# Kernel optimization log

Hardware: AMD Instinct MI355X
Metric: run time of the kernel (lower is better)

## Reference

```python
import jax, jax.numpy as jnp
import numpy as np

N, E, D, L, G, C = 20000, 320000, 512, 6, 64, 10
EPS = 1e-5


def setup_inputs() -> dict:
    key = jax.random.key(0)
    ks = jax.random.split(key, 8)
    s = 0.05  # small init scale to keep activations sane across 6 layers
    x = jax.random.normal(ks[0], (N, D), jnp.float32)
    edge_index = jax.random.randint(ks[1], (2, E), 0, N, jnp.int32)
    batch = jnp.sort(jax.random.randint(ks[2], (N,), 0, G, jnp.int32))
    W_rel = jax.random.normal(ks[3], (L, D, D), jnp.float32) * s
    b_rel = jnp.zeros((L, D), jnp.float32)
    W_root = jax.random.normal(ks[4], (L, D, D), jnp.float32) * s
    gamma = jnp.ones((L, D), jnp.float32)
    beta = jnp.zeros((L, D), jnp.float32)
    lin_w = jax.random.normal(ks[5], (D, C), jnp.float32) * s
    lin_b = jnp.zeros((C,), jnp.float32)
    return {"x": x, "edge_index": edge_index, "batch": batch,
            "W_rel": W_rel, "b_rel": b_rel, "W_root": W_root,
            "gamma": gamma, "beta": beta, "lin_w": lin_w, "lin_b": lin_b}


def reference(x, edge_index, batch, W_rel, b_rel, W_root, gamma, beta, lin_w, lin_b):
    # PyG GraphConv (aggr='add'): out = segment_sum(x[src] -> dst) @ W_rel + b_rel + x @ W_root
    src, dst = edge_index[0], edge_index[1]
    n = x.shape[0]
    for l in range(W_rel.shape[0]):  # 6 structurally identical layers
        agg = jax.ops.segment_sum(x[src], dst, num_segments=n)  # [N, D]
        h = agg @ W_rel[l] + b_rel[l] + x @ W_root[l]
        # BatchNorm1d in training mode: biased batch statistics over nodes
        mu = jnp.mean(h, axis=0)
        var = jnp.mean(jnp.square(h - mu), axis=0)
        x = jax.nn.relu((h - mu) * jax.lax.rsqrt(var + EPS) * gamma[l] + beta[l])
    # global_mean_pool over per-node graph ids
    sums = jax.ops.segment_sum(x, batch, num_segments=G)              # [G, D]
    counts = jax.ops.segment_sum(jnp.ones((n,), x.dtype), batch, num_segments=G)
    pooled = sums / jnp.maximum(counts, 1.0)[:, None]
    return pooled @ lin_w + lin_b  # [G, C]
```

## Files before the change

kernel.cpp:

```cpp
#include <hip/hip_runtime.h>


typedef unsigned short u16;
typedef unsigned int u32;
typedef __attribute__((ext_vector_type(8))) short bf16x8;
typedef __attribute__((ext_vector_type(16))) float f32x16;
typedef __attribute__((ext_vector_type(2))) float f32x2;

#define DFEAT 512
#define KDIM 1024
#define NLAYER 6
#define NGRAPH 64
#define NCLS 10
#define BN_EPS 1e-5f
#define NBUCKET 1024

__device__ __forceinline__ float bf_lo(u32 u) { union { u32 i; float f; } v; v.i = u << 16; return v.f; }
__device__ __forceinline__ float bf_hi(u32 u) { union { u32 i; float f; } v; v.i = u & 0xFFFF0000u; return v.f; }
__device__ __forceinline__ u16 f2bf(float f) {
  union { float f; u32 i; } v; v.f = f;
  u32 r = v.i + 0x7FFFu + ((v.i >> 16) & 1u);
  return (u16)(r >> 16);
}
__device__ __forceinline__ u32 pack2(float lo, float hi) {
  return (u32)f2bf(lo) | ((u32)f2bf(hi) << 16);
}

__device__ __forceinline__ void gload_lds16(const u16* g, u16* lds_base) {
  __builtin_amdgcn_global_load_lds(
      (const __attribute__((address_space(1))) u32*)g,
      (__attribute__((address_space(3))) u32*)lds_base, 16, 0, 0);
}

__global__ void prep_kernel(const int* __restrict__ ei, int* __restrict__ counts, int E,
                            const float* __restrict__ Wrel, const float* __restrict__ Wroot,
                            u16* __restrict__ Wt,
                            const float* __restrict__ x, u16* __restrict__ A, int M,
                            int histB, int wB) {
  __shared__ float tile[64][65];
  int b = blockIdx.x;
  int tid = threadIdx.x;
  if (b < histB) {
    int e = b * 256 + tid;
    if (e < E) atomicAdd(&counts[ei[E + e]], 1);
  } else if (b < histB + wB) {
    int t = b - histB;
    int l = t >> 7;
    int tt = t & 127;
    int k0 = (tt >> 3) << 6;
    int n0 = (tt & 7) << 6;
    int rr = tid >> 4;
    int c4 = (tid & 15) << 2;
#pragma unroll
    for (int i = 0; i < 4; i++) {
      int k = k0 + i * 16 + rr;
      const float* src = (k < DFEAT)
          ? &Wrel[((size_t)l * DFEAT + k) * DFEAT + n0 + c4]
          : &Wroot[((size_t)l * DFEAT + (k - DFEAT)) * DFEAT + n0 + c4];
      float4 v = *(const float4*)src;
      float* d = &tile[i * 16 + rr][c4];
      d[0] = v.x; d[1] = v.y; d[2] = v.z; d[3] = v.w;
    }
    __syncthreads();
    int nr = tid >> 3;
    int kc = (tid & 7) << 3;
#pragma unroll
    for (int i = 0; i < 2; i++) {
      int nl = i * 32 + nr;
      uint4 o;
      o.x = pack2(tile[kc + 0][nl], tile[kc + 1][nl]);
      o.y = pack2(tile[kc + 2][nl], tile[kc + 3][nl]);
      o.z = pack2(tile[kc + 4][nl], tile[kc + 5][nl]);
      o.w = pack2(tile[kc + 6][nl], tile[kc + 7][nl]);
      *(uint4*)&Wt[(size_t)(l * DFEAT + n0 + nl) * KDIM + k0 + kc] = o;
    }
  } else {
    int idx = (b - histB - wB) * 256 + tid;
    int row = idx >> 7;
    int c4 = (idx & 127) * 4;
    if (row < M) {
      float4 v = *(const float4*)&x[(size_t)row * DFEAT + c4];
      uint2 o; o.x = pack2(v.x, v.y); o.y = pack2(v.z, v.w);
      *(uint2*)&A[(size_t)row * KDIM + DFEAT + c4] = o;
    }
  }
}

__global__ __launch_bounds__(1024) void dscan_kernel(const int* __restrict__ counts,
                                                     int* __restrict__ base0,
                                                     int* __restrict__ bcur,
                                                     int* __restrict__ edgebase,
                                                     int* __restrict__ row_ptr2, int n) {
  __shared__ int hist[NBUCKET];
  __shared__ int part[NBUCKET];
  int tid = threadIdx.x;
  hist[tid] = 0;
  __syncthreads();
  for (int i = tid; i < n; i += 1024) {
    int d = counts[i]; if (d > NBUCKET - 1) d = NBUCKET - 1;
    atomicAdd(&hist[d], 1);
  }
  __syncthreads();
  int c = hist[tid];
  part[tid] = c; __syncthreads();
  int x = c;
  for (int off = 1; off < NBUCKET; off <<= 1) {
    int t = (tid >= off) ? part[tid - off] : 0;
    __syncthreads();
    x += t; part[tid] = x;
    __syncthreads();
  }
  base0[tid] = x - c;
  bcur[tid] = x - c;
  int w = c * tid;
  part[tid] = w; __syncthreads();
  int y = w;
  for (int off = 1; off < NBUCKET; off <<= 1) {
    int t = (tid >= off) ? part[tid - off] : 0;
    __syncthreads();
    y += t; part[tid] = y;
    __syncthreads();
  }
  edgebase[tid] = y - w;
  if (tid == NBUCKET - 1) row_ptr2[n] = y;
}

__global__ __launch_bounds__(256) void rank_kernel(const int* __restrict__ counts,
                                                   const int* __restrict__ base0,
                                                   int* __restrict__ bcur,
                                                   const int* __restrict__ edgebase,
                                                   int* __restrict__ perm,
                                                   int* __restrict__ row_ptr2,
                                                   int* __restrict__ cursor2, int n) {
  __shared__ int hb[NBUCKET];
  __shared__ int hstart[NBUCKET];
  int tid = threadIdx.x;
  for (int d = tid; d < NBUCKET; d += 256) hb[d] = 0;
  __syncthreads();
  int row = blockIdx.x * 256 + tid;
  bool valid = (row < n);
  int deg = 0, j = 0;
  if (valid) {
    deg = counts[row]; if (deg > NBUCKET - 1) deg = NBUCKET - 1;
    j = atomicAdd(&hb[deg], 1);
  }
  __syncthreads();
  for (int d = tid; d < NBUCKET; d += 256) {
    int c = hb[d];
    hstart[d] = c ? atomicAdd(&bcur[d], c) : 0;
  }
  __syncthreads();
  if (valid) {
    int rnk = hstart[deg] + j;
    int jj = rnk - base0[deg];
    int v = edgebase[deg] + jj * deg;
    perm[rnk] = row;
    row_ptr2[rnk] = v;
    cursor2[row] = v;
  }
}

__global__ void scatter_kernel(const int* __restrict__ ei, int* __restrict__ cursor2,
                               int* __restrict__ csr2, int E) {
  int e = blockIdx.x * 256 + threadIdx.x;
  if (e < E) {
    int d = ei[E + e];
    int pos = atomicAdd(&cursor2[d], 1);
    csr2[pos] = ei[e];
  }
}

template <bool FUSED>
__device__ __forceinline__ void acc8(uint4 v, const f32x2* sc, const f32x2* sh, f32x2* a) {
  f32x2 t0 = {bf_lo(v.x), bf_hi(v.x)};
  f32x2 t1 = {bf_lo(v.y), bf_hi(v.y)};
  f32x2 t2 = {bf_lo(v.z), bf_hi(v.z)};
  f32x2 t3 = {bf_lo(v.w), bf_hi(v.w)};
  if constexpr (FUSED) {
    f32x2 z = {0.f, 0.f};
    a[0] += __builtin_elementwise_max(t0 * sc[0] + sh[0], z);
    a[1] += __builtin_elementwise_max(t1 * sc[1] + sh[1], z);
    a[2] += __builtin_elementwise_max(t2 * sc[2] + sh[2], z);
    a[3] += __builtin_elementwise_max(t3 * sc[3] + sh[3], z);
  } else {
    a[0] += t0; a[1] += t1; a[2] += t2; a[3] += t3;
  }
}

#define GCAP 1536
template <bool FUSED>
__global__ __launch_bounds__(256) void gather_kernel(u16* __restrict__ A,
                                                     const u16* __restrict__ Hb,
                                                     const float* __restrict__ sums,
                                                     const float* __restrict__ gamma,
                                                     const float* __restrict__ beta,
                                                     const int* __restrict__ row_ptr2,
                                                     const int* __restrict__ csr2,
                                                     const int* __restrict__ perm,
                                                     int n, float invN) {
  __shared__ int sidx[GCAP];
  int b = blockIdx.x;
  int slice = b & 7;
  int nGrp = (n + 31) >> 5;
  int grp = nGrp - 1 - (b >> 3);
  int tid = threadIdx.x;
  int r0 = grp * 32;
  int rend = (r0 + 32 < n) ? (r0 + 32) : n;
  int wbeg = row_ptr2[r0], wend = row_ptr2[rend];
  int cnt = wend - wbeg;
  bool lds_ok = (cnt <= GCAP);
  if (lds_ok)
    for (int t = tid; t < cnt; t += 256) sidx[t] = csr2[wbeg + t];
  __syncthreads();

  int wid = tid >> 6, lane = tid & 63;
  int dsub = lane >> 3, fl = lane & 7;
  int rnk = r0 + wid * 8 + dsub;
  if (rnk >= n) return;
  int dst = perm[rnk];
  int cc = slice * 64 + fl * 8;
  f32x2 sc2[4], sh2[4];
  if constexpr (FUSED) {
#pragma unroll
    for (int j = 0; j < 8; j++) {
      int c = cc + j;
      float mu = sums[c] * invN;
      float var = sums[DFEAT + c] * invN - mu * mu;
      float s = gamma[c] * rsqrtf(var + BN_EPS);
      sc2[j >> 1][j & 1] = s;
      sh2[j >> 1][j & 1] = beta[c] - mu * s;
    }
    uint4 h = *(const uint4*)&Hb[(size_t)dst * DFEAT + cc];
    f32x2 z = {0.f, 0.f};
    f32x2 e0 = __builtin_elementwise_max((f32x2){bf_lo(h.x), bf_hi(h.x)} * sc2[0] + sh2[0], z);
    f32x2 e1 = __builtin_elementwise_max((f32x2){bf_lo(h.y), bf_hi(h.y)} * sc2[1] + sh2[1], z);
    f32x2 e2 = __builtin_elementwise_max((f32x2){bf_lo(h.z), bf_hi(h.z)} * sc2[2] + sh2[2], z);
    f32x2 e3 = __builtin_elementwise_max((f32x2){bf_lo(h.w), bf_hi(h.w)} * sc2[3] + sh2[3], z);
    uint4 o;
    o.x = pack2(e0[0], e0[1]); o.y = pack2(e1[0], e1[1]);
    o.z = pack2(e2[0], e2[1]); o.w = pack2(e3[0], e3[1]);
    *(uint4*)&A[(size_t)dst * KDIM + DFEAT + cc] = o;
  }
  const u16* Sx = FUSED ? (Hb + cc) : (A + DFEAT + cc);
  const size_t RS = FUSED ? DFEAT : KDIM;
  int db = row_ptr2[rnk], de = row_ptr2[rnk + 1];
  f32x2 a[4] = {};
  if (lds_ok) {
    int e = db - wbeg, ee = de - wbeg;
    for (; e + 7 < ee; e += 8) {
      int s0 = sidx[e + 0], s1 = sidx[e + 1], s2 = sidx[e + 2], s3 = sidx[e + 3];
      int s4 = sidx[e + 4], s5 = sidx[e + 5], s6 = sidx[e + 6], s7 = sidx[e + 7];
      uint4 v0 = *(const uint4*)&Sx[(size_t)s0 * RS];
      uint4 v1 = *(const uint4*)&Sx[(size_t)s1 * RS];
      uint4 v2 = *(const uint4*)&Sx[(size_t)s2 * RS];
      uint4 v3 = *(const uint4*)&Sx[(size_t)s3 * RS];
      uint4 v4 = *(const uint4*)&Sx[(size_t)s4 * RS];
      uint4 v5 = *(const uint4*)&Sx[(size_t)s5 * RS];
      uint4 v6 = *(const uint4*)&Sx[(size_t)s6 * RS];
      uint4 v7 = *(const uint4*)&Sx[(size_t)s7 * RS];
      acc8<FUSED>(v0, sc2, sh2, a); acc8<FUSED>(v1, sc2, sh2, a);
      acc8<FUSED>(v2, sc2, sh2, a); acc8<FUSED>(v3, sc2, sh2, a);
      acc8<FUSED>(v4, sc2, sh2, a); acc8<FUSED>(v5, sc2, sh2, a);
      acc8<FUSED>(v6, sc2, sh2, a); acc8<FUSED>(v7, sc2, sh2, a);
    }
    for (; e < ee; ++e) {
      uint4 v = *(const uint4*)&Sx[(size_t)sidx[e] * RS];
      acc8<FUSED>(v, sc2, sh2, a);
    }
  } else {
    for (int e = db; e < de; ++e) {
      uint4 v = *(const uint4*)&Sx[(size_t)csr2[e] * RS];
      acc8<FUSED>(v, sc2, sh2, a);
    }
  }
  uint4 o;
  o.x = pack2(a[0][0], a[0][1]); o.y = pack2(a[1][0], a[1][1]);
  o.z = pack2(a[2][0], a[2][1]); o.w = pack2(a[3][0], a[3][1]);
  *(uint4*)&A[(size_t)dst * KDIM + cc] = o;
}

#define BM 128
#define BN 128
#define BK 64
#define CSTR 132
#define BUFSZ (BM * BK + BN * BK)
__global__ __launch_bounds__(256, 2) void gemm_kernel(const u16* __restrict__ A,
                                                      const u16* __restrict__ Bt,
                                                      const float* __restrict__ bias,
                                                      u16* __restrict__ Hb,
                                                      float* __restrict__ sums, int M) {
  const int lin = blockIdx.x;
  const int bx = ((lin >> 5) << 3) + (lin & 7);
  const int by = (lin >> 3) & 3;
  const int m0 = bx * BM;
  if (m0 >= M) return;
  const int n0 = by * BN;

  __shared__ u16 smem[2 * BUFSZ];
  __shared__ float sred[2 * BN];
  const int tid = threadIdx.x;
  const int wid = tid >> 6, lane = tid & 63;
  const int wm = wid >> 1, wn = wid & 1;
  const int l31 = lane & 31, half = lane >> 5;

  if (tid < 2 * BN) sred[tid] = 0.f;

  const int dr = lane >> 3;
  const int gcol = ((lane & 7) ^ dr) * 8;
  int arow[4], brow[4];
#pragma unroll
  for (int t = 0; t < 4; t++) {
    int r = wid * 32 + t * 8 + dr;
    int ar = m0 + r; if (ar >= M) ar = M - 1;
    arow[t] = ar;
    brow[t] = n0 + r;
  }

  f32x16 acc[2][2] = {};

#pragma unroll
  for (int t = 0; t < 4; t++) {
    gload_lds16(&A[(size_t)arow[t] * KDIM + gcol], &smem[(wid * 32 + t * 8) * BK]);
    gload_lds16(&Bt[(size_t)brow[t] * KDIM + gcol], &smem[BM * BK + (wid * 32 + t * 8) * BK]);
  }
  __syncthreads();

  const int NIT = KDIM / BK;
  for (int it = 0; it < NIT; ++it) {
    const int cur = it & 1;
    if (it + 1 < NIT) {
      const int k1 = (it + 1) * BK;
      u16* Asn = &smem[(cur ^ 1) * BUFSZ];
      u16* Bsn = Asn + BM * BK;
#pragma unroll
      for (int t = 0; t < 4; t++) {
        gload_lds16(&A[(size_t)arow[t] * KDIM + k1 + gcol], &Asn[(wid * 32 + t * 8) * BK]);
        gload_lds16(&Bt[(size_t)brow[t] * KDIM + k1 + gcol], &Bsn[(wid * 32 + t * 8) * BK]);
      }
    }
    const u16* Asc = &smem[cur * BUFSZ];
    const u16* Bsc = Asc + BM * BK;
#pragma unroll
    for (int ks = 0; ks < 4; ks++) {
      int slot = ((ks * 2 + half) ^ (l31 & 7)) * 8;
      bf16x8 a0 = *(const bf16x8*)&Asc[(wm * 64 + l31) * BK + slot];
      bf16x8 a1 = *(const bf16x8*)&Asc[(wm * 64 + 32 + l31) * BK + slot];
      bf16x8 b0 = *(const bf16x8*)&Bsc[(wn * 64 + l31) * BK + slot];
      bf16x8 b1 = *(const bf16x8*)&Bsc[(wn * 64 + 32 + l31) * BK + slot];
      acc[0][0] = __builtin_amdgcn_mfma_f32_32x32x16_bf16(a0, b0, acc[0][0], 0, 0, 0);
      acc[0][1] = __builtin_amdgcn_mfma_f32_32x32x16_bf16(a0, b1, acc[0][1], 0, 0, 0);
      acc[1][0] = __builtin_amdgcn_mfma_f32_32x32x16_bf16(a1, b0, acc[1][0], 0, 0, 0);
      acc[1][1] = __builtin_amdgcn_mfma_f32_32x32x16_bf16(a1, b1, acc[1][1], 0, 0, 0);
    }
    __syncthreads();
  }

#pragma unroll
  for (int nt = 0; nt < 2; nt++) {
    int colt = wn * 64 + nt * 32 + l31;
    float bv = bias[n0 + colt];
    float s = 0.f, s2 = 0.f;
#pragma unroll
    for (int mt = 0; mt < 2; mt++) {
      int rbase = wm * 64 + mt * 32 + half * 4;
#pragma unroll
      for (int reg = 0; reg < 16; reg++) {
        int rowt = rbase + (reg & 3) + 8 * (reg >> 2);
        float v = acc[mt][nt][reg] + bv;
        smem[rowt * CSTR + colt] = f2bf(v);
        if (m0 + rowt < M) { s += v; s2 += v * v; }
      }
    }
    s  += __shfl_xor(s, 32);
    s2 += __shfl_xor(s2, 32);
    if (half == 0) {
      atomicAdd(&sred[colt], s);
      atomicAdd(&sred[BN + colt], s2);
    }
  }
  __syncthreads();

  const int rsub = tid >> 4;
  const int c8 = (tid & 15) * 8;
#pragma unroll
  for (int it = 0; it < 8; it++) {
    int rowt = it * 16 + rsub;
    int grow = m0 + rowt;
    if (grow < M) {
      uint4 v = *(const uint4*)&smem[rowt * CSTR + c8];
      *(uint4*)&Hb[(size_t)grow * DFEAT + n0 + c8] = v;
    }
  }
  if (tid < BN) {
    atomicAdd(&sums[n0 + tid], sred[tid]);
    atomicAdd(&sums[DFEAT + n0 + tid], sred[BN + tid]);
  }
}

__device__ __forceinline__ int lower_bound_dev(const int* a, int n, int v) {
  int lo = 0, hi = n;
  while (lo < hi) { int mid = (lo + hi) >> 1; if (a[mid] < v) lo = mid + 1; else hi = mid; }
  return lo;
}

__global__ __launch_bounds__(1024) void pool_kernel(const u16* __restrict__ Hb,
                                                    const float* __restrict__ sums,
                                                    const float* __restrict__ gamma,
                                                    const float* __restrict__ beta,
                                                    const int* __restrict__ batch,
                                                    float* __restrict__ pooled, int n, float invN) {
  __shared__ float red[DFEAT];
  int g = blockIdx.x;
  int tid = threadIdx.x;
  if (tid < DFEAT) red[tid] = 0.f;
  int lo = lower_bound_dev(batch, n, g);
  int hi = lower_bound_dev(batch, n, g + 1);
  int rowOff = tid >> 6, lane = tid & 63;
  int c0 = lane * 8;
  float sc[8], sh[8];
#pragma unroll
  for (int j = 0; j < 8; j++) {
    int c = c0 + j;
    float mu = sums[c] * invN;
    float var = sums[DFEAT + c] * invN - mu * mu;
    float s = gamma[c] * rsqrtf(var + BN_EPS);
    sc[j] = s;
    sh[j] = beta[c] - mu * s;
  }
  float a[8] = {};
  for (int r = lo + rowOff; r < hi; r += 16) {
    uint4 v = *(const uint4*)&Hb[(size_t)r * DFEAT + c0];
    float e0 = bf_lo(v.x), e1 = bf_hi(v.x), e2 = bf_lo(v.y), e3 = bf_hi(v.y);
    float e4 = bf_lo(v.z), e5 = bf_hi(v.z), e6 = bf_lo(v.w), e7 = bf_hi(v.w);
    a[0] += fmaxf(e0 * sc[0] + sh[0], 0.f); a[1] += fmaxf(e1 * sc[1] + sh[1], 0.f);
    a[2] += fmaxf(e2 * sc[2] + sh[2], 0.f); a[3] += fmaxf(e3 * sc[3] + sh[3], 0.f);
    a[4] += fmaxf(e4 * sc[4] + sh[4], 0.f); a[5] += fmaxf(e5 * sc[5] + sh[5], 0.f);
    a[6] += fmaxf(e6 * sc[6] + sh[6], 0.f); a[7] += fmaxf(e7 * sc[7] + sh[7], 0.f);
  }
  __syncthreads();
#pragma unroll
  for (int j = 0; j < 8; j++) atomicAdd(&red[c0 + j], a[j]);
  __syncthreads();
  if (tid < DFEAT) pooled[g * DFEAT + tid] = red[tid] / fmaxf((float)(hi - lo), 1.0f);
}

__global__ __launch_bounds__(64) void final_kernel(const float* __restrict__ pooled,
                                                   const float* __restrict__ lin_w,
                                                   const float* __restrict__ lin_b,
                                                   float* __restrict__ out) {
  int g = blockIdx.x;
  int lane = threadIdx.x;
  float acc[NCLS] = {};
  float4 p0 = *(const float4*)&pooled[g * DFEAT + lane * 8];
  float4 p1 = *(const float4*)&pooled[g * DFEAT + lane * 8 + 4];
  float pv[8] = {p0.x, p0.y, p0.z, p0.w, p1.x, p1.y, p1.z, p1.w};
#pragma unroll
  for (int j = 0; j < 8; j++) {
    int k = lane * 8 + j;
#pragma unroll
    for (int c = 0; c < NCLS; c++) acc[c] += pv[j] * lin_w[k * NCLS + c];
  }
#pragma unroll
  for (int off = 32; off > 0; off >>= 1)
#pragma unroll
    for (int c = 0; c < NCLS; c++) acc[c] += __shfl_down(acc[c], off);
  if (lane == 0)
#pragma unroll
    for (int c = 0; c < NCLS; c++) out[g * NCLS + c] = acc[c] + lin_b[c];
}

extern "C" void kernel_launch(void* const* d_in, const int* in_sizes, int n_in,
                              void* d_out, int out_size, void* d_ws, size_t ws_size,
                              hipStream_t stream) {
  const float* x      = (const float*)d_in[0];
  const int*   ei     = (const int*)d_in[1];
  const int*   batch  = (const int*)d_in[2];
  const float* W_rel  = (const float*)d_in[3];
  const float* b_rel  = (const float*)d_in[4];
  const float* W_root = (const float*)d_in[5];
  const float* gamma  = (const float*)d_in[6];
  const float* beta   = (const float*)d_in[7];
  const float* lin_w  = (const float*)d_in[8];
  const float* lin_b  = (const float*)d_in[9];
  float* out = (float*)d_out;

  const int N = in_sizes[0] / DFEAT;
  const int E = in_sizes[1] / 2;

  char* p = (char*)d_ws;
  u16*   A        = (u16*)p;    p += (size_t)N * KDIM * 2;
  u16*   Hb       = (u16*)p;    p += (size_t)N * DFEAT * 2;
  u16*   Wt       = (u16*)p;    p += (size_t)NLAYER * DFEAT * KDIM * 2;
  int*   row_ptr2 = (int*)p;    p += ((size_t)(N + 1) * 4 + 15) / 16 * 16;
  int*   counts   = (int*)p;    p += (size_t)N * 4;
  int*   cursor2  = (int*)p;    p += (size_t)N * 4;
  int*   perm     = (int*)p;    p += (size_t)N * 4;
  int*   csr2     = (int*)p;    p += (size_t)E * 4;
  int*   base0    = (int*)p;    p += (size_t)NBUCKET * 4;
  int*   bcur     = (int*)p;    p += (size_t)NBUCKET * 4;
  int*   edgebase = (int*)p;    p += (size_t)NBUCKET * 4;
  float* sums     = (float*)p;  p += (size_t)NLAYER * 2 * DFEAT * 4;
  float* pooled   = (float*)p;  p += (size_t)NGRAPH * DFEAT * 4;

  const float invN = 1.0f / (float)N;

  hipMemsetAsync(counts, 0, (size_t)N * 4, stream);
  hipMemsetAsync(sums, 0, (size_t)NLAYER * 2 * DFEAT * 4, stream);

  const int histB = (E + 255) / 256;
  const int wB = NLAYER * 128;
  const int xB = (N * 128 + 255) / 256;
  prep_kernel<<<histB + wB + xB, 256, 0, stream>>>(ei, counts, E, W_rel, W_root, Wt,
                                                   x, A, N, histB, wB);
  dscan_kernel<<<1, 1024, 0, stream>>>(counts, base0, bcur, edgebase, row_ptr2, N);
  rank_kernel<<<(N + 255) / 256, 256, 0, stream>>>(counts, base0, bcur, edgebase,
                                                   perm, row_ptr2, cursor2, N);
  scatter_kernel<<<(E + 255) / 256, 256, 0, stream>>>(ei, cursor2, csr2, E);

  const int ngrp8 = ((N + 31) / 32) * 8;
  const int gtiles = (((N + BM - 1) / BM + 7) / 8) * 8 * 4;

  for (int l = 0; l < NLAYER; ++l) {
    float* sums_l = sums + (size_t)l * 2 * DFEAT;
    if (l == 0)
      gather_kernel<false><<<ngrp8, 256, 0, stream>>>(A, Hb, nullptr, nullptr, nullptr,
                                                      row_ptr2, csr2, perm, N, invN);
    else
      gather_kernel<true><<<ngrp8, 256, 0, stream>>>(A, Hb,
          sums + (size_t)(l - 1) * 2 * DFEAT,
          gamma + (size_t)(l - 1) * DFEAT, beta + (size_t)(l - 1) * DFEAT,
          row_ptr2, csr2, perm, N, invN);
    gemm_kernel<<<gtiles, 256, 0, stream>>>(A, Wt + (size_t)l * DFEAT * KDIM,
                                            b_rel + (size_t)l * DFEAT, Hb, sums_l, N);
  }

  pool_kernel<<<NGRAPH, 1024, 0, stream>>>(Hb, sums + (size_t)(NLAYER - 1) * 2 * DFEAT,
                                           gamma + (size_t)(NLAYER - 1) * DFEAT,
                                           beta + (size_t)(NLAYER - 1) * DFEAT,
                                           batch, pooled, N, invN);
  final_kernel<<<NGRAPH, 64, 0, stream>>>(pooled, lin_w, lin_b, out);
}
```

Before: 621.7 us.

## Deepen GEMM prefetch to two stages and fuse final linear into pool kernel

```diff
diff --git a/kernel.cpp b/kernel.cpp
--- a/kernel.cpp
+++ b/kernel.cpp
@@ -316,28 +316,30 @@
     brow[t] = n0 + r;
   }
 
+  auto STAGE = [&](int pb, int kt) {
+    const int k0 = kt * BK;
+    u16* As = &smem[pb * BUFSZ];
+    u16* Bs = As + BM * BK;
+#pragma unroll
+    for (int t = 0; t < 4; t++)
+      gload_lds16(&A[(size_t)arow[t] * KDIM + k0 + gcol], &As[(wid * 32 + t * 8) * BK]);
+#pragma unroll
+    for (int t = 0; t < 4; t++)
+      gload_lds16(&Bt[(size_t)brow[t] * KDIM + k0 + gcol], &Bs[(wid * 32 + t * 8) * BK]);
+  };
+
   f32x16 acc[2][2] = {};
 
-#pragma unroll
-  for (int t = 0; t < 4; t++) {
-    gload_lds16(&A[(size_t)arow[t] * KDIM + gcol], &smem[(wid * 32 + t * 8) * BK]);
-    gload_lds16(&Bt[(size_t)brow[t] * KDIM + gcol], &smem[BM * BK + (wid * 32 + t * 8) * BK]);
-  }
-  __syncthreads();
+  STAGE(0, 0);
+  STAGE(1, 1);
+  asm volatile("s_waitcnt vmcnt(8)" ::: "memory");
+  __builtin_amdgcn_sched_barrier(0);
+  __builtin_amdgcn_s_barrier();
+  __builtin_amdgcn_sched_barrier(0);
 
   const int NIT = KDIM / BK;
   for (int it = 0; it < NIT; ++it) {
     const int cur = it & 1;
-    if (it + 1 < NIT) {
-      const int k1 = (it + 1) * BK;
-      u16* Asn = &smem[(cur ^ 1) * BUFSZ];
-      u16* Bsn = Asn + BM * BK;
-#pragma unroll
-      for (int t = 0; t < 4; t++) {
-        gload_lds16(&A[(size_t)arow[t] * KDIM + k1 + gcol], &Asn[(wid * 32 + t * 8) * BK]);
-        gload_lds16(&Bt[(size_t)brow[t] * KDIM + k1 + gcol], &Bsn[(wid * 32 + t * 8) * BK]);
-      }
-    }
     const u16* Asc = &smem[cur * BUFSZ];
     const u16* Bsc = Asc + BM * BK;
 #pragma unroll
@@ -352,7 +354,20 @@
       acc[1][0] = __builtin_amdgcn_mfma_f32_32x32x16_bf16(a1, b0, acc[1][0], 0, 0, 0);
       acc[1][1] = __builtin_amdgcn_mfma_f32_32x32x16_bf16(a1, b1, acc[1][1], 0, 0, 0);
     }
-    __syncthreads();
+    __builtin_amdgcn_sched_barrier(0);
+    __builtin_amdgcn_s_barrier();
+    __builtin_amdgcn_sched_barrier(0);
+    if (it + 2 < NIT) {
+      STAGE(cur, it + 2);
+      asm volatile("s_waitcnt vmcnt(8)" ::: "memory");
+    } else if (it + 2 == NIT) {
+      asm volatile("s_waitcnt vmcnt(0)" ::: "memory");
+    }
+    __builtin_amdgcn_sched_barrier(0);
+    if (it + 1 < NIT) {
+      __builtin_amdgcn_s_barrier();
+      __builtin_amdgcn_sched_barrier(0);
+    }
   }
 
 #pragma unroll
@@ -408,11 +423,15 @@
                                                     const float* __restrict__ gamma,
                                                     const float* __restrict__ beta,
                                                     const int* __restrict__ batch,
-                                                    float* __restrict__ pooled, int n, float invN) {
+                                                    const float* __restrict__ lin_w,
+                                                    const float* __restrict__ lin_b,
+                                                    float* __restrict__ out, int n, float invN) {
   __shared__ float red[DFEAT];
+  __shared__ float outc[NCLS];
   int g = blockIdx.x;
   int tid = threadIdx.x;
   if (tid < DFEAT) red[tid] = 0.f;
+  if (tid >= DFEAT && tid < DFEAT + NCLS) outc[tid - DFEAT] = 0.f;
   int lo = lower_bound_dev(batch, n, g);
   int hi = lower_bound_dev(batch, n, g + 1);
   int rowOff = tid >> 6, lane = tid & 63;
@@ -441,32 +460,22 @@
 #pragma unroll
   for (int j = 0; j < 8; j++) atomicAdd(&red[c0 + j], a[j]);
   __syncthreads();
-  if (tid < DFEAT) pooled[g * DFEAT + tid] = red[tid] / fmaxf((float)(hi - lo), 1.0f);
-}
-
-__global__ __launch_bounds__(64) void final_kernel(const float* __restrict__ pooled,
-                                                   const float* __restrict__ lin_w,
-                                                   const float* __restrict__ lin_b,
-                                                   float* __restrict__ out) {
-  int g = blockIdx.x;
-  int lane = threadIdx.x;
-  float acc[NCLS] = {};
-  float4 p0 = *(const float4*)&pooled[g * DFEAT + lane * 8];
-  float4 p1 = *(const float4*)&pooled[g * DFEAT + lane * 8 + 4];
-  float pv[8] = {p0.x, p0.y, p0.z, p0.w, p1.x, p1.y, p1.z, p1.w};
-#pragma unroll
-  for (int j = 0; j < 8; j++) {
-    int k = lane * 8 + j;
-#pragma unroll
-    for (int c = 0; c < NCLS; c++) acc[c] += pv[j] * lin_w[k * NCLS + c];
-  }
-#pragma unroll
-  for (int off = 32; off > 0; off >>= 1)
-#pragma unroll
-    for (int c = 0; c < NCLS; c++) acc[c] += __shfl_down(acc[c], off);
-  if (lane == 0)
-#pragma unroll
-    for (int c = 0; c < NCLS; c++) out[g * NCLS + c] = acc[c] + lin_b[c];
+  float invCnt = 1.0f / fmaxf((float)(hi - lo), 1.0f);
+  if (tid < DFEAT) {
+    float pv = red[tid] * invCnt;
+    float pc[NCLS];
+#pragma unroll
+    for (int c = 0; c < NCLS; c++) pc[c] = pv * lin_w[tid * NCLS + c];
+#pragma unroll
+    for (int off = 32; off > 0; off >>= 1)
+#pragma unroll
+      for (int c = 0; c < NCLS; c++) pc[c] += __shfl_down(pc[c], off);
+    if ((tid & 63) == 0)
+#pragma unroll
+      for (int c = 0; c < NCLS; c++) atomicAdd(&outc[c], pc[c]);
+  }
+  __syncthreads();
+  if (tid < NCLS) out[g * NCLS + tid] = outc[tid] + lin_b[tid];
 }
 
 extern "C" void kernel_launch(void* const* d_in, const int* in_sizes, int n_in,
@@ -500,7 +509,6 @@
   int*   bcur     = (int*)p;    p += (size_t)NBUCKET * 4;
   int*   edgebase = (int*)p;    p += (size_t)NBUCKET * 4;
   float* sums     = (float*)p;  p += (size_t)NLAYER * 2 * DFEAT * 4;
-  float* pooled   = (float*)p;  p += (size_t)NGRAPH * DFEAT * 4;
 
   const float invN = 1.0f / (float)N;
 
@@ -537,6 +545,5 @@
   pool_kernel<<<NGRAPH, 1024, 0, stream>>>(Hb, sums + (size_t)(NLAYER - 1) * 2 * DFEAT,
                                            gamma + (size_t)(NLAYER - 1) * DFEAT,
                                            beta + (size_t)(NLAYER - 1) * DFEAT,
-                                           batch, pooled, N, invN);
-  final_kernel<<<NGRAPH, 64, 0, stream>>>(pooled, lin_w, lin_b, out);
-}
+                                           batch, lin_w, lin_b, out, N, invN);
+}
```

Result: no change. 614.0 us (-1.2%).
